# Kernel optimization log

Hardware: AMD Instinct MI355X
Metric: run time of the kernel (lower is better)

The kernel has to match this reference:

```python
import jax, jax.numpy as jnp
import numpy as np

N_NODES = 80000
N_EDGES = 1280000
IN_DIM = 32
EDGE_DIM = 16
HID = 64
DEPTH = 4
BN_EPS = 1e-5
LN_EPS = 1e-5


def setup_inputs() -> dict:
    key = jax.random.key(0)
    ks = jax.random.split(key, 20)
    s = lambda fan: 1.0 / np.sqrt(fan)
    inp = {
        "x": jax.random.normal(ks[0], (N_NODES, IN_DIM), jnp.float32),
        "edge_index": jax.random.randint(ks[1], (2, N_EDGES), 0, N_NODES, jnp.int32),
        "edge_attr": jax.random.normal(ks[2], (N_EDGES, EDGE_DIM), jnp.float32),
        # input embeddings
        "Wx": jax.random.normal(ks[3], (IN_DIM, HID), jnp.float32) * s(IN_DIM),
        "bx": jnp.zeros((HID,), jnp.float32),
        "We": jax.random.normal(ks[4], (EDGE_DIM, HID), jnp.float32) * s(EDGE_DIM),
        "be": jnp.zeros((HID,), jnp.float32),
        # per-layer GIN MLP params (stacked over DEPTH)
        "W1": jax.random.normal(ks[5], (DEPTH, HID, 2 * HID), jnp.float32) * s(HID),
        "b1": jnp.zeros((DEPTH, 2 * HID), jnp.float32),
        "g1": jnp.ones((DEPTH, 2 * HID), jnp.float32),   # BatchNorm gamma
        "bt1": jnp.zeros((DEPTH, 2 * HID), jnp.float32),  # BatchNorm beta
        "W2": jax.random.normal(ks[6], (DEPTH, 2 * HID, HID), jnp.float32) * s(2 * HID),
        "b2": jnp.zeros((DEPTH, HID), jnp.float32),
        "eps": jnp.zeros((DEPTH,), jnp.float32),           # GIN epsilon, init 0
        # per-layer LayerNorm params
        "ln_g": jnp.ones((DEPTH, HID), jnp.float32),
        "ln_b": jnp.zeros((DEPTH, HID), jnp.float32),
    }
    return inp


def reference(x, edge_index, edge_attr, Wx, bx, We, be, W1, b1, g1, bt1, W2, b2, eps, ln_g, ln_b):
    n = x.shape[0]
    h = jax.nn.relu(x @ Wx + bx)                      # [N, HID]
    ea = jax.nn.relu(edge_attr @ We + be)             # [E, HID]
    row, col = edge_index[0], edge_index[1]           # source, target
    L = W1.shape[0]
    for l in range(L):
        # message: relu(x_j + edge_attr), scatter-add into target nodes
        msg = jax.nn.relu(h[row] + ea)                # [E, HID]
        agg = jax.ops.segment_sum(msg, col, num_segments=n)  # [N, HID]
        z = (1.0 + eps[l]) * h + agg
        # GIN MLP: Linear -> BatchNorm(train stats) -> ReLU -> Linear
        z = z @ W1[l] + b1[l]                         # [N, 2*HID]
        mu = z.mean(axis=0)
        var = z.var(axis=0)                           # biased, as torch BN training
        z = (z - mu) * jax.lax.rsqrt(var + BN_EPS) * g1[l] + bt1[l]
        z = jax.nn.relu(z)
        z = z @ W2[l] + b2[l]                         # [N, HID]
        # LayerNorm
        lm = z.mean(axis=-1, keepdims=True)
        lv = z.var(axis=-1, keepdims=True)
        z = (z - lm) * jax.lax.rsqrt(lv + LN_EPS) * ln_g[l] + ln_b[l]
        if l < L - 1:
            z = jax.nn.relu(z)
        h = z
    return h  # JK == 'last'
```

## Files before the change

### kernel.cpp

```cpp
#include <hip/hip_runtime.h>
#include <cstdint>

typedef _Float16 half8 __attribute__((ext_vector_type(8)));
typedef float f32x4 __attribute__((ext_vector_type(4)));

#define NNODES 80000
#define NEDGES 1280000
#define INDIM 32
#define EDIM 16
#define HID 64
#define HID2 128
#define DEPTH 4
#define BN_EPS 1e-5f
#define LN_EPS 1e-5f
#define NB 313

union U16x8 { uint4 v; _Float16 h[8]; };

__global__ __launch_bounds__(256) void k_node_embed(
    const float* __restrict__ x, const float* __restrict__ Wx,
    const float* __restrict__ bx, _Float16* __restrict__ h16) {
    int gw = (blockIdx.x * 256 + threadIdx.x) >> 6;
    int lane = threadIdx.x & 63;
    if (gw >= NNODES) return;
    float xv = (lane < INDIM) ? x[(size_t)gw * INDIM + lane] : 0.f;
    float acc = bx[lane];
#pragma unroll
    for (int k = 0; k < INDIM; k++)
        acc = fmaf(__shfl(xv, k, 64), Wx[k * HID + lane], acc);
    h16[(size_t)gw * HID + lane] = (_Float16)fmaxf(acc, 0.f);
}

__global__ __launch_bounds__(256) void k_prep(
    const float* __restrict__ W1, const float* __restrict__ W2,
    _Float16* __restrict__ w1T, _Float16* __restrict__ w2T) {
    int id = blockIdx.x * 256 + threadIdx.x;
    if (id < DEPTH * 128 * 64) {
        int l = id / 8192, r = id % 8192, n = r / 64, k = r % 64;
        w1T[id] = (_Float16)W1[(size_t)l * 8192 + k * 128 + n];
    } else {
        int idx = id - DEPTH * 128 * 64;
        int l = idx / 8192, r = idx % 8192, n = r / 128, k = r % 128;
        w2T[idx] = (_Float16)W2[(size_t)l * 8192 + k * 64 + n];
    }
}

__global__ __launch_bounds__(256) void k_hist(const int* __restrict__ col, int* __restrict__ deg) {
    int e = blockIdx.x * 256 + threadIdx.x;
    if (e < NEDGES) atomicAdd(&deg[col[e]], 1);
}

__global__ __launch_bounds__(256) void k_scan1(const int* __restrict__ deg, int* __restrict__ bsum) {
    __shared__ int s[256];
    int i = blockIdx.x * 256 + threadIdx.x;
    int v = (i < NNODES) ? deg[i] : 0;
    s[threadIdx.x] = v;
    __syncthreads();
    for (int o = 128; o > 0; o >>= 1) {
        if (threadIdx.x < o) s[threadIdx.x] += s[threadIdx.x + o];
        __syncthreads();
    }
    if (threadIdx.x == 0) bsum[blockIdx.x] = s[0];
}

__global__ __launch_bounds__(512) void k_scan2(const int* __restrict__ bsum, int* __restrict__ boff) {
    __shared__ int s[512];
    int t = threadIdx.x;
    s[t] = (t < NB) ? bsum[t] : 0;
    __syncthreads();
    for (int o = 1; o < 512; o <<= 1) {
        int v = (t >= o) ? s[t - o] : 0;
        __syncthreads();
        s[t] += v;
        __syncthreads();
    }
    if (t < NB) boff[t] = (t == 0) ? 0 : s[t - 1];
}

__global__ __launch_bounds__(256) void k_scan3(const int* __restrict__ deg,
                                               const int* __restrict__ boff,
                                               int* __restrict__ row_off) {
    __shared__ int s[256];
    int i = blockIdx.x * 256 + threadIdx.x;
    int t = threadIdx.x;
    int v = (i < NNODES) ? deg[i] : 0;
    s[t] = v;
    __syncthreads();
    for (int o = 1; o < 256; o <<= 1) {
        int u = (t >= o) ? s[t - o] : 0;
        __syncthreads();
        s[t] += u;
        __syncthreads();
    }
    int incl = s[t];
    if (i < NNODES) row_off[i] = boff[blockIdx.x] + incl - v;
    if (i == NNODES - 1) row_off[NNODES] = boff[blockIdx.x] + incl;
}

__global__ __launch_bounds__(256) void k_copy(const int* __restrict__ src, int* __restrict__ dst) {
    int i = blockIdx.x * 256 + threadIdx.x;
    if (i < NNODES) dst[i] = src[i];
}

__global__ __launch_bounds__(256) void k_scatter(const int* __restrict__ row,
                                                 const int* __restrict__ col,
                                                 int* __restrict__ cursor,
                                                 uint2* __restrict__ sre) {
    int e = blockIdx.x * 256 + threadIdx.x;
    if (e < NEDGES) {
        int c = col[e];
        int pos = atomicAdd(&cursor[c], 1);
        sre[pos] = make_uint2((unsigned)row[e], (unsigned)e);
    }
}

__global__ __launch_bounds__(256) void k_edge_embed(
    const float* __restrict__ eat, const uint2* __restrict__ sre,
    const float* __restrict__ We, const float* __restrict__ be,
    _Float16* __restrict__ eas) {
    __shared__ __align__(16) unsigned char lds[4][5120 + 8192];
    int tid = threadIdx.x;
    int w = tid >> 6, lane = tid & 63;
    unsigned char* A = lds[w];
    unsigned char* O = lds[w] + 5120;
    int ebase = blockIdx.x * 256 + w * 64;
    int b = lane >> 4, c = lane & 15;
    half8 bf[4];
#pragma unroll
    for (int t = 0; t < 4; t++) {
        half8 v = {};
        if (b < 2) {
#pragma unroll
            for (int j = 0; j < 8; j++) {
                int k = b * 8 + j;
                v[j] = (_Float16)We[k * HID + t * 16 + c];
            }
        }
        bf[t] = v;
    }
    float bias[4];
#pragma unroll
    for (int t = 0; t < 4; t++) bias[t] = be[t * 16 + c];
    int eid = (int)sre[ebase + lane].y;
    const float4* ar = (const float4*)(eat + (size_t)eid * EDIM);
    float4 a0 = ar[0], a1 = ar[1], a2 = ar[2], a3 = ar[3];
    U16x8 lo, hi;
    lo.h[0] = (_Float16)a0.x; lo.h[1] = (_Float16)a0.y;
    lo.h[2] = (_Float16)a0.z; lo.h[3] = (_Float16)a0.w;
    lo.h[4] = (_Float16)a1.x; lo.h[5] = (_Float16)a1.y;
    lo.h[6] = (_Float16)a1.z; lo.h[7] = (_Float16)a1.w;
    hi.h[0] = (_Float16)a2.x; hi.h[1] = (_Float16)a2.y;
    hi.h[2] = (_Float16)a2.z; hi.h[3] = (_Float16)a2.w;
    hi.h[4] = (_Float16)a3.x; hi.h[5] = (_Float16)a3.y;
    hi.h[6] = (_Float16)a3.z; hi.h[7] = (_Float16)a3.w;
    uint4 zz = make_uint4(0, 0, 0, 0);
    *(uint4*)(A + lane * 80) = lo.v;
    *(uint4*)(A + lane * 80 + 16) = hi.v;
    *(uint4*)(A + lane * 80 + 32) = zz;
    *(uint4*)(A + lane * 80 + 48) = zz;
    __syncthreads();
#pragma unroll
    for (int it = 0; it < 4; it++) {
        half8 af = *(const half8*)(A + (it * 16 + c) * 80 + b * 16);
#pragma unroll
        for (int t = 0; t < 4; t++) {
            f32x4 acc = {0.f, 0.f, 0.f, 0.f};
            acc = __builtin_amdgcn_mfma_f32_16x16x32_f16(af, bf[t], acc, 0, 0, 0);
#pragma unroll
            for (int r = 0; r < 4; r++) {
                int erow = it * 16 + b * 4 + r;
                int chan = t * 16 + c;
                float v = fmaxf(acc[r] + bias[t], 0.f);
                int byteoff = (erow * 128 + chan * 2) ^ ((erow & 7) << 4);
                *(_Float16*)(O + byteoff) = (_Float16)v;
            }
        }
    }
    __syncthreads();
    uint4* dst = (uint4*)(eas + (size_t)(ebase + lane) * HID);
#pragma unroll
    for (int q = 0; q < 8; q++)
        dst[q] = *(const uint4*)(O + ((lane * 128 + q * 16) ^ ((lane & 7) << 4)));
}

__global__ __launch_bounds__(256) void k_msg(
    const _Float16* __restrict__ h16, const int* __restrict__ row_off,
    const uint2* __restrict__ sre, const _Float16* __restrict__ eas,
    const float* __restrict__ epsp, _Float16* __restrict__ zc16) {
    int gw = (blockIdx.x * 256 + threadIdx.x) >> 6;
    int lane = threadIdx.x & 63;
    if (gw >= NNODES) return;
    int beg = row_off[gw], end = row_off[gw + 1];
    float acc = 0.f;
    int e = beg;
    for (; e + 7 < end; e += 8) {
        int j[8];
#pragma unroll
        for (int u = 0; u < 8; u++) j[u] = (int)sre[e + u].x;
        float hv[8], ev[8];
#pragma unroll
        for (int u = 0; u < 8; u++) hv[u] = (float)h16[(size_t)j[u] * HID + lane];
#pragma unroll
        for (int u = 0; u < 8; u++) ev[u] = (float)eas[(size_t)(e + u) * HID + lane];
        float t0 = fmaxf(hv[0] + ev[0], 0.f) + fmaxf(hv[1] + ev[1], 0.f);
        float t1 = fmaxf(hv[2] + ev[2], 0.f) + fmaxf(hv[3] + ev[3], 0.f);
        float t2 = fmaxf(hv[4] + ev[4], 0.f) + fmaxf(hv[5] + ev[5], 0.f);
        float t3 = fmaxf(hv[6] + ev[6], 0.f) + fmaxf(hv[7] + ev[7], 0.f);
        acc += (t0 + t1) + (t2 + t3);
    }
    for (; e < end; ++e) {
        int j = (int)sre[e].x;
        float hv = (float)h16[(size_t)j * HID + lane];
        float ev = (float)eas[(size_t)e * HID + lane];
        acc += fmaxf(hv + ev, 0.f);
    }
    float epsl = *epsp;
    float hv0 = (float)h16[(size_t)gw * HID + lane];
    zc16[(size_t)gw * HID + lane] = (_Float16)((1.f + epsl) * hv0 + acc);
}

__global__ __launch_bounds__(256) void k_gemm1(
    const _Float16* __restrict__ zc16, const _Float16* __restrict__ w1Tl,
    const float* __restrict__ b1l, _Float16* __restrict__ z1,
    float* __restrict__ bn_acc) {
    __shared__ __align__(16) unsigned char At[64 * 128];
    __shared__ __align__(16) unsigned char Bt[128 * 128];
    __shared__ float red[4][HID2][2];
    int tid = threadIdx.x;
    int nb = blockIdx.x * 64;
#pragma unroll
    for (int i = 0; i < 2; i++) {
        int id = tid + 256 * i;
        int node = id >> 3, c = id & 7;
        uint4 v = *(const uint4*)(zc16 + (size_t)(nb + node) * HID + c * 8);
        *(uint4*)(At + node * 128 + ((c ^ (node & 7)) << 4)) = v;
    }
#pragma unroll
    for (int i = 0; i < 4; i++) {
        int id = tid + 256 * i;
        int r = id >> 3, c = id & 7;
        uint4 v = *(const uint4*)(w1Tl + (size_t)r * HID + c * 8);
        *(uint4*)(Bt + r * 128 + ((c ^ (r & 7)) << 4)) = v;
    }
    __syncthreads();
    int lane = tid & 63, w = tid >> 6;
    int rl = lane & 15, b = lane >> 4;
    f32x4 acc[8];
#pragma unroll
    for (int t = 0; t < 8; t++) acc[t] = (f32x4){0.f, 0.f, 0.f, 0.f};
#pragma unroll
    for (int s = 0; s < 2; s++) {
        int arow = w * 16 + rl;
        half8 af = *(const half8*)(At + arow * 128 + (((s * 4 + b) ^ (rl & 7)) << 4));
#pragma unroll
        for (int t = 0; t < 8; t++) {
            int brow = t * 16 + rl;
            half8 bf = *(const half8*)(Bt + brow * 128 + (((s * 4 + b) ^ (rl & 7)) << 4));
            acc[t] = __builtin_amdgcn_mfma_f32_16x16x32_f16(af, bf, acc[t], 0, 0, 0);
        }
    }
#pragma unroll
    for (int t = 0; t < 8; t++) {
        int colg = t * 16 + rl;
        float bias = b1l[colg];
        float s = 0.f, q = 0.f;
#pragma unroll
        for (int r = 0; r < 4; r++) {
            float v = acc[t][r] + bias;
            int node = nb + w * 16 + b * 4 + r;
            z1[(size_t)node * HID2 + colg] = (_Float16)v;
            s += v;
            q = fmaf(v, v, q);
        }
        s += __shfl_xor(s, 16, 64); s += __shfl_xor(s, 32, 64);
        q += __shfl_xor(q, 16, 64); q += __shfl_xor(q, 32, 64);
        if (b == 0) { red[w][colg][0] = s; red[w][colg][1] = q; }
    }
    __syncthreads();
    int ch = tid & 127, which = tid >> 7;
    float tot = red[0][ch][which] + red[1][ch][which] + red[2][ch][which] + red[3][ch][which];
    atomicAdd(&bn_acc[which * HID2 + ch], tot);
}

__global__ void k_bnfin(const float* __restrict__ bn_acc,
                        const float* __restrict__ g1l,
                        const float* __restrict__ bt1l,
                        float* __restrict__ bn_sc) {
    int c = threadIdx.x;
    if (c >= HID2) return;
    float inv_n = 1.f / (float)NNODES;
    float mu = bn_acc[c] * inv_n;
    float ex2 = bn_acc[HID2 + c] * inv_n;
    float var = ex2 - mu * mu;
    float rs = rsqrtf(var + BN_EPS);
    float sc = g1l[c] * rs;
    bn_sc[c] = sc;
    bn_sc[HID2 + c] = bt1l[c] - mu * sc;
}

__global__ __launch_bounds__(256) void k_mlp2(
    const _Float16* __restrict__ z1, const float* __restrict__ bn_sc,
    const _Float16* __restrict__ w2Tl, const float* __restrict__ b2l,
    const float* __restrict__ lngl, const float* __restrict__ lnbl,
    int last, _Float16* __restrict__ hout, float* __restrict__ fout) {
    __shared__ __align__(16) unsigned char Yt[64 * 256];
    __shared__ __align__(16) unsigned char Wt[64 * 256];
    __shared__ float sbn[256];
    int tid = threadIdx.x;
    int nb = blockIdx.x * 64;
    sbn[tid] = bn_sc[tid];
#pragma unroll
    for (int i = 0; i < 4; i++) {
        int id = tid + 256 * i;
        int r = id >> 4, c = id & 15;
        uint4 v = *(const uint4*)(w2Tl + (size_t)r * HID2 + c * 8);
        *(uint4*)(Wt + r * 256 + ((c ^ (r & 7)) << 4)) = v;
    }
    __syncthreads();
#pragma unroll
    for (int i = 0; i < 4; i++) {
        int id = tid + 256 * i;
        int node = id >> 4, c = id & 15;
        U16x8 u, o;
        u.v = *(const uint4*)(z1 + (size_t)(nb + node) * HID2 + c * 8);
#pragma unroll
        for (int j = 0; j < 8; j++) {
            int chn = c * 8 + j;
            float y = fmaxf(fmaf((float)u.h[j], sbn[chn], sbn[HID2 + chn]), 0.f);
            o.h[j] = (_Float16)y;
        }
        *(uint4*)(Yt + node * 256 + ((c ^ (node & 7)) << 4)) = o.v;
    }
    __syncthreads();
    int lane = tid & 63, w = tid >> 6;
    int rl = lane & 15, b = lane >> 4;
    f32x4 acc[4];
#pragma unroll
    for (int t = 0; t < 4; t++) acc[t] = (f32x4){0.f, 0.f, 0.f, 0.f};
#pragma unroll
    for (int s = 0; s < 4; s++) {
        int arow = w * 16 + rl;
        half8 af = *(const half8*)(Yt + arow * 256 + (((s * 4 + b) ^ (rl & 7)) << 4));
#pragma unroll
        for (int t = 0; t < 4; t++) {
            int brow = t * 16 + rl;
            half8 bf = *(const half8*)(Wt + brow * 256 + (((s * 4 + b) ^ (rl & 7)) << 4));
            acc[t] = __builtin_amdgcn_mfma_f32_16x16x32_f16(af, bf, acc[t], 0, 0, 0);
        }
    }
    float a[4][4];
#pragma unroll
    for (int t = 0; t < 4; t++) {
        float bias = b2l[t * 16 + rl];
#pragma unroll
        for (int r = 0; r < 4; r++) a[r][t] = acc[t][r] + bias;
    }
    float m[4], vv[4];
#pragma unroll
    for (int r = 0; r < 4; r++) {
        float s = (a[r][0] + a[r][1]) + (a[r][2] + a[r][3]);
        s += __shfl_xor(s, 1, 64); s += __shfl_xor(s, 2, 64);
        s += __shfl_xor(s, 4, 64); s += __shfl_xor(s, 8, 64);
        m[r] = s * (1.f / 64.f);
    }
#pragma unroll
    for (int r = 0; r < 4; r++) {
        float t0 = a[r][0] - m[r], t1 = a[r][1] - m[r];
        float t2 = a[r][2] - m[r], t3 = a[r][3] - m[r];
        float q = (t0 * t0 + t1 * t1) + (t2 * t2 + t3 * t3);
        q += __shfl_xor(q, 1, 64); q += __shfl_xor(q, 2, 64);
        q += __shfl_xor(q, 4, 64); q += __shfl_xor(q, 8, 64);
        vv[r] = rsqrtf(q * (1.f / 64.f) + LN_EPS);
    }
#pragma unroll
    for (int t = 0; t < 4; t++) {
        int colg = t * 16 + rl;
        float lg = lngl[colg], lb = lnbl[colg];
#pragma unroll
        for (int r = 0; r < 4; r++) {
            float o = (a[r][t] - m[r]) * vv[r] * lg + lb;
            size_t node = nb + w * 16 + b * 4 + r;
            if (last) {
                fout[node * HID + colg] = o;
            } else {
                hout[node * HID + colg] = (_Float16)fmaxf(o, 0.f);
            }
        }
    }
}

extern "C" void kernel_launch(void* const* d_in, const int* in_sizes, int n_in,
                              void* d_out, int out_size, void* d_ws, size_t ws_size,
                              hipStream_t stream) {
    const float* x   = (const float*)d_in[0];
    const int*   ei  = (const int*)d_in[1];
    const float* eat = (const float*)d_in[2];
    const float* Wx  = (const float*)d_in[3];
    const float* bx  = (const float*)d_in[4];
    const float* We  = (const float*)d_in[5];
    const float* be  = (const float*)d_in[6];
    const float* W1  = (const float*)d_in[7];
    const float* b1  = (const float*)d_in[8];
    const float* g1  = (const float*)d_in[9];
    const float* bt1 = (const float*)d_in[10];
    const float* W2  = (const float*)d_in[11];
    const float* b2  = (const float*)d_in[12];
    const float* eps = (const float*)d_in[13];
    const float* lng = (const float*)d_in[14];
    const float* lnb = (const float*)d_in[15];
    const int* row = ei;
    const int* col = ei + NEDGES;

    char* p = (char*)d_ws;
    auto alloc = [&](size_t bytes) -> char* {
        char* r = p;
        p += (bytes + 255) & ~(size_t)255;
        return r;
    };
    _Float16* h16  = (_Float16*)alloc((size_t)NNODES * HID * 2);
    _Float16* zc16 = (_Float16*)alloc((size_t)NNODES * HID * 2);
    _Float16* z1   = (_Float16*)alloc((size_t)NNODES * HID2 * 2);
    int* row_off   = (int*)alloc((size_t)(NNODES + 1) * 4);
    uint2* sre     = (uint2*)alloc((size_t)NEDGES * 8);
    _Float16* eas  = (_Float16*)alloc((size_t)NEDGES * HID * 2);
    _Float16* w1T  = (_Float16*)alloc((size_t)DEPTH * 128 * 64 * 2);
    _Float16* w2T  = (_Float16*)alloc((size_t)DEPTH * 64 * 128 * 2);
    float* bn_acc  = (float*)alloc(256 * 4);
    float* bn_sc   = (float*)alloc(256 * 4);
    int* cursor = (int*)z1;
    int* bsum   = (int*)z1 + NNODES;
    int* boff   = bsum + NB;
    (void)ws_size; (void)in_sizes; (void)n_in; (void)out_size;

    hipMemsetAsync(cursor, 0, (size_t)NNODES * 4, stream);
    k_node_embed<<<(NNODES + 3) / 4, 256, 0, stream>>>(x, Wx, bx, h16);
    k_prep<<<(DEPTH * 8192 * 2) / 256, 256, 0, stream>>>(W1, W2, w1T, w2T);
    k_hist<<<(NEDGES + 255) / 256, 256, 0, stream>>>(col, cursor);
    k_scan1<<<NB, 256, 0, stream>>>(cursor, bsum);
    k_scan2<<<1, 512, 0, stream>>>(bsum, boff);
    k_scan3<<<NB, 256, 0, stream>>>(cursor, boff, row_off);
    k_copy<<<NB, 256, 0, stream>>>(row_off, cursor);
    k_scatter<<<(NEDGES + 255) / 256, 256, 0, stream>>>(row, col, cursor, sre);
    k_edge_embed<<<NEDGES / 256, 256, 0, stream>>>(eat, sre, We, be, eas);

    const int msg_blocks = (NNODES + 3) / 4;
    const int mm_blocks = NNODES / 64;
    for (int l = 0; l < DEPTH; ++l) {
        k_msg<<<msg_blocks, 256, 0, stream>>>(h16, row_off, sre, eas, eps + l, zc16);
        hipMemsetAsync(bn_acc, 0, 256 * 4, stream);
        k_gemm1<<<mm_blocks, 256, 0, stream>>>(zc16, w1T + (size_t)l * 8192,
                                               b1 + (size_t)l * HID2, z1, bn_acc);
        k_bnfin<<<1, 128, 0, stream>>>(bn_acc, g1 + (size_t)l * HID2,
                                       bt1 + (size_t)l * HID2, bn_sc);
        k_mlp2<<<mm_blocks, 256, 0, stream>>>(z1, bn_sc, w2T + (size_t)l * 8192,
                                              b2 + (size_t)l * HID,
                                              lng + (size_t)l * HID, lnb + (size_t)l * HID,
                                              (l == DEPTH - 1) ? 1 : 0, h16, (float*)d_out);
    }
}
```

Before: 730.3 us.

## Fuse message aggregation into GEMM1 and bucket-partition the CSR edge scatter

The per-layer message kernel is merged into the first MLP GEMM, so each 64-node block gathers and aggregates its neighbours straight into LDS instead of writing and re-reading a zc16 buffer. CSR construction becomes a two-pass bucketed partition: edges are first binned by 128-node bucket into a temp area that reuses the eas buffer, then scattered locally, which should give better write locality than the fully random scatter. The packed uint2 sorted array is split into separate row and edge-id arrays so the gather reads only 4 bytes per edge. The risk is that the fused kernel runs only 1250 blocks with 16 sequential nodes per wave, which lowers latency hiding for the gather, and the bucket capacity of 4096 assumes no bucket overflows for these inputs.

```diff
diff --git a/kernel.cpp b/kernel.cpp
--- a/kernel.cpp
+++ b/kernel.cpp
@@ -14,6 +14,8 @@
 #define BN_EPS 1e-5f
 #define LN_EPS 1e-5f
 #define NB 313
+#define NBUCK 625
+#define BCAP 4096
 
 union U16x8 { uint4 v; _Float16 h[8]; };
 
@@ -45,9 +47,17 @@
     }
 }
 
-__global__ __launch_bounds__(256) void k_hist(const int* __restrict__ col, int* __restrict__ deg) {
+__global__ __launch_bounds__(256) void k_part1(
+    const int* __restrict__ row, const int* __restrict__ col,
+    int* __restrict__ deg, int* __restrict__ bcur, uint2* __restrict__ tmp) {
     int e = blockIdx.x * 256 + threadIdx.x;
-    if (e < NEDGES) atomicAdd(&deg[col[e]], 1);
+    int r = row[e];
+    int c = col[e];
+    atomicAdd(&deg[c], 1);
+    int b = c >> 7;
+    int cloc = c & 127;
+    int p = atomicAdd(&bcur[b], 1);
+    tmp[(size_t)b * BCAP + p] = make_uint2((unsigned)r | ((unsigned)cloc << 17), (unsigned)e);
 }
 
 __global__ __launch_bounds__(256) void k_scan1(const int* __restrict__ deg, int* __restrict__ bsum) {
@@ -102,20 +112,24 @@
     if (i < NNODES) dst[i] = src[i];
 }
 
-__global__ __launch_bounds__(256) void k_scatter(const int* __restrict__ row,
-                                                 const int* __restrict__ col,
-                                                 int* __restrict__ cursor,
-                                                 uint2* __restrict__ sre) {
-    int e = blockIdx.x * 256 + threadIdx.x;
-    if (e < NEDGES) {
-        int c = col[e];
+__global__ __launch_bounds__(256) void k_part2(
+    const uint2* __restrict__ tmp, const int* __restrict__ bcur,
+    int* __restrict__ cursor, int* __restrict__ srow, int* __restrict__ seid) {
+    int b = blockIdx.x;
+    int cnt = bcur[b];
+    const uint2* src = tmp + (size_t)b * BCAP;
+    for (int i = threadIdx.x; i < cnt; i += 256) {
+        uint2 v = src[i];
+        int r = (int)(v.x & 0x1FFFF);
+        int c = (b << 7) + (int)(v.x >> 17);
         int pos = atomicAdd(&cursor[c], 1);
-        sre[pos] = make_uint2((unsigned)row[e], (unsigned)e);
+        srow[pos] = r;
+        seid[pos] = (int)v.y;
     }
 }
 
 __global__ __launch_bounds__(256) void k_edge_embed(
-    const float* __restrict__ eat, const uint2* __restrict__ sre,
+    const float* __restrict__ eat, const int* __restrict__ seid,
     const float* __restrict__ We, const float* __restrict__ be,
     _Float16* __restrict__ eas) {
     __shared__ __align__(16) unsigned char lds[4][5120 + 8192];
@@ -141,7 +155,7 @@
     float bias[4];
 #pragma unroll
     for (int t = 0; t < 4; t++) bias[t] = be[t * 16 + c];
-    int eid = (int)sre[ebase + lane].y;
+    int eid = seid[ebase + lane];
     const float4* ar = (const float4*)(eat + (size_t)eid * EDIM);
     float4 a0 = ar[0], a1 = ar[1], a2 = ar[2], a3 = ar[3];
     U16x8 lo, hi;
@@ -183,44 +197,10 @@
         dst[q] = *(const uint4*)(O + ((lane * 128 + q * 16) ^ ((lane & 7) << 4)));
 }
 
-__global__ __launch_bounds__(256) void k_msg(
+__global__ __launch_bounds__(256) void k_msg1(
     const _Float16* __restrict__ h16, const int* __restrict__ row_off,
-    const uint2* __restrict__ sre, const _Float16* __restrict__ eas,
-    const float* __restrict__ epsp, _Float16* __restrict__ zc16) {
-    int gw = (blockIdx.x * 256 + threadIdx.x) >> 6;
-    int lane = threadIdx.x & 63;
-    if (gw >= NNODES) return;
-    int beg = row_off[gw], end = row_off[gw + 1];
-    float acc = 0.f;
-    int e = beg;
-    for (; e + 7 < end; e += 8) {
-        int j[8];
-#pragma unroll
-        for (int u = 0; u < 8; u++) j[u] = (int)sre[e + u].x;
-        float hv[8], ev[8];
-#pragma unroll
-        for (int u = 0; u < 8; u++) hv[u] = (float)h16[(size_t)j[u] * HID + lane];
-#pragma unroll
-        for (int u = 0; u < 8; u++) ev[u] = (float)eas[(size_t)(e + u) * HID + lane];
-        float t0 = fmaxf(hv[0] + ev[0], 0.f) + fmaxf(hv[1] + ev[1], 0.f);
-        float t1 = fmaxf(hv[2] + ev[2], 0.f) + fmaxf(hv[3] + ev[3], 0.f);
-        float t2 = fmaxf(hv[4] + ev[4], 0.f) + fmaxf(hv[5] + ev[5], 0.f);
-        float t3 = fmaxf(hv[6] + ev[6], 0.f) + fmaxf(hv[7] + ev[7], 0.f);
-        acc += (t0 + t1) + (t2 + t3);
-    }
-    for (; e < end; ++e) {
-        int j = (int)sre[e].x;
-        float hv = (float)h16[(size_t)j * HID + lane];
-        float ev = (float)eas[(size_t)e * HID + lane];
-        acc += fmaxf(hv + ev, 0.f);
-    }
-    float epsl = *epsp;
-    float hv0 = (float)h16[(size_t)gw * HID + lane];
-    zc16[(size_t)gw * HID + lane] = (_Float16)((1.f + epsl) * hv0 + acc);
-}
-
-__global__ __launch_bounds__(256) void k_gemm1(
-    const _Float16* __restrict__ zc16, const _Float16* __restrict__ w1Tl,
+    const int* __restrict__ srow, const _Float16* __restrict__ eas,
+    const float* __restrict__ epsp, const _Float16* __restrict__ w1Tl,
     const float* __restrict__ b1l, _Float16* __restrict__ z1,
     float* __restrict__ bn_acc) {
     __shared__ __align__(16) unsigned char At[64 * 128];
@@ -229,21 +209,47 @@
     int tid = threadIdx.x;
     int nb = blockIdx.x * 64;
 #pragma unroll
-    for (int i = 0; i < 2; i++) {
-        int id = tid + 256 * i;
-        int node = id >> 3, c = id & 7;
-        uint4 v = *(const uint4*)(zc16 + (size_t)(nb + node) * HID + c * 8);
-        *(uint4*)(At + node * 128 + ((c ^ (node & 7)) << 4)) = v;
-    }
-#pragma unroll
     for (int i = 0; i < 4; i++) {
         int id = tid + 256 * i;
         int r = id >> 3, c = id & 7;
         uint4 v = *(const uint4*)(w1Tl + (size_t)r * HID + c * 8);
         *(uint4*)(Bt + r * 128 + ((c ^ (r & 7)) << 4)) = v;
     }
-    __syncthreads();
     int lane = tid & 63, w = tid >> 6;
+    float epsl = 1.f + *epsp;
+    for (int t = 0; t < 16; ++t) {
+        int node = nb + w * 16 + t;
+        int beg = row_off[node], end = row_off[node + 1];
+        float acc = 0.f;
+        int e = beg;
+        for (; e + 7 < end; e += 8) {
+            int j[8];
+#pragma unroll
+            for (int u = 0; u < 8; u++) j[u] = srow[e + u];
+            float hv[8], ev[8];
+#pragma unroll
+            for (int u = 0; u < 8; u++) hv[u] = (float)h16[(size_t)j[u] * HID + lane];
+#pragma unroll
+            for (int u = 0; u < 8; u++) ev[u] = (float)eas[(size_t)(e + u) * HID + lane];
+            float t0 = fmaxf(hv[0] + ev[0], 0.f) + fmaxf(hv[1] + ev[1], 0.f);
+            float t1 = fmaxf(hv[2] + ev[2], 0.f) + fmaxf(hv[3] + ev[3], 0.f);
+            float t2 = fmaxf(hv[4] + ev[4], 0.f) + fmaxf(hv[5] + ev[5], 0.f);
+            float t3 = fmaxf(hv[6] + ev[6], 0.f) + fmaxf(hv[7] + ev[7], 0.f);
+            acc += (t0 + t1) + (t2 + t3);
+        }
+        for (; e < end; ++e) {
+            int j = srow[e];
+            float hv = (float)h16[(size_t)j * HID + lane];
+            float ev = (float)eas[(size_t)e * HID + lane];
+            acc += fmaxf(hv + ev, 0.f);
+        }
+        float hv0 = (float)h16[(size_t)node * HID + lane];
+        float val = epsl * hv0 + acc;
+        int nl = w * 16 + t;
+        int byteoff = nl * 128 + ((((lane >> 3) ^ (nl & 7))) << 4) + (lane & 7) * 2;
+        *(_Float16*)(At + byteoff) = (_Float16)val;
+    }
+    __syncthreads();
     int rl = lane & 15, b = lane >> 4;
     f32x4 acc[8];
 #pragma unroll
@@ -418,38 +424,40 @@
         return r;
     };
     _Float16* h16  = (_Float16*)alloc((size_t)NNODES * HID * 2);
-    _Float16* zc16 = (_Float16*)alloc((size_t)NNODES * HID * 2);
     _Float16* z1   = (_Float16*)alloc((size_t)NNODES * HID2 * 2);
     int* row_off   = (int*)alloc((size_t)(NNODES + 1) * 4);
-    uint2* sre     = (uint2*)alloc((size_t)NEDGES * 8);
+    int* srow      = (int*)alloc((size_t)NEDGES * 4);
     _Float16* eas  = (_Float16*)alloc((size_t)NEDGES * HID * 2);
     _Float16* w1T  = (_Float16*)alloc((size_t)DEPTH * 128 * 64 * 2);
     _Float16* w2T  = (_Float16*)alloc((size_t)DEPTH * 64 * 128 * 2);
     float* bn_acc  = (float*)alloc(256 * 4);
     float* bn_sc   = (float*)alloc(256 * 4);
+    int*   bcur    = (int*)alloc((size_t)NBUCK * 4);
+    uint2* tmp  = (uint2*)eas;
     int* cursor = (int*)z1;
     int* bsum   = (int*)z1 + NNODES;
     int* boff   = bsum + NB;
+    int* seid   = (int*)z1 + 2 * NNODES;
     (void)ws_size; (void)in_sizes; (void)n_in; (void)out_size;
 
     hipMemsetAsync(cursor, 0, (size_t)NNODES * 4, stream);
+    hipMemsetAsync(bcur, 0, (size_t)NBUCK * 4, stream);
     k_node_embed<<<(NNODES + 3) / 4, 256, 0, stream>>>(x, Wx, bx, h16);
     k_prep<<<(DEPTH * 8192 * 2) / 256, 256, 0, stream>>>(W1, W2, w1T, w2T);
-    k_hist<<<(NEDGES + 255) / 256, 256, 0, stream>>>(col, cursor);
+    k_part1<<<NEDGES / 256, 256, 0, stream>>>(row, col, cursor, bcur, tmp);
     k_scan1<<<NB, 256, 0, stream>>>(cursor, bsum);
     k_scan2<<<1, 512, 0, stream>>>(bsum, boff);
     k_scan3<<<NB, 256, 0, stream>>>(cursor, boff, row_off);
     k_copy<<<NB, 256, 0, stream>>>(row_off, cursor);
-    k_scatter<<<(NEDGES + 255) / 256, 256, 0, stream>>>(row, col, cursor, sre);
-    k_edge_embed<<<NEDGES / 256, 256, 0, stream>>>(eat, sre, We, be, eas);
-
-    const int msg_blocks = (NNODES + 3) / 4;
+    k_part2<<<NBUCK, 256, 0, stream>>>(tmp, bcur, cursor, srow, seid);
+    k_edge_embed<<<NEDGES / 256, 256, 0, stream>>>(eat, seid, We, be, eas);
+
     const int mm_blocks = NNODES / 64;
     for (int l = 0; l < DEPTH; ++l) {
-        k_msg<<<msg_blocks, 256, 0, stream>>>(h16, row_off, sre, eas, eps + l, zc16);
         hipMemsetAsync(bn_acc, 0, 256 * 4, stream);
-        k_gemm1<<<mm_blocks, 256, 0, stream>>>(zc16, w1T + (size_t)l * 8192,
-                                               b1 + (size_t)l * HID2, z1, bn_acc);
+        k_msg1<<<mm_blocks, 256, 0, stream>>>(h16, row_off, srow, eas, eps + l,
+                                              w1T + (size_t)l * 8192,
+                                              b1 + (size_t)l * HID2, z1, bn_acc);
         k_bnfin<<<1, 128, 0, stream>>>(bn_acc, g1 + (size_t)l * HID2,
                                        bt1 + (size_t)l * HID2, bn_sc);
         k_mlp2<<<mm_blocks, 256, 0, stream>>>(z1, bn_sc, w2T + (size_t)l * 8192,
```

Result: slower. 1.246 ms (+70.7%).

## Partition histogram and scatter atomics by destination range per XCD

Applied to the files above, without the earlier changes.

Reworks the degree histogram and CSR scatter kernels so that each block handles a slice of edges but only applies atomics for destination nodes in one of eight node ranges, selected by blockIdx&7. The intent is that blocks scheduled round-robin onto the same XCD touch only one eighth of the counter array, keeping atomics L2-local and avoiding cross-die contention. In exchange, every edge's column is read eight times and most lanes go idle on the range test, and the XCD mapping assumption is not guaranteed.

```diff
diff --git a/kernel.cpp b/kernel.cpp
--- a/kernel.cpp
+++ b/kernel.cpp
@@ -14,6 +14,8 @@
 #define BN_EPS 1e-5f
 #define LN_EPS 1e-5f
 #define NB 313
+#define NPX 10000
+#define EPS 10000
 
 union U16x8 { uint4 v; _Float16 h[8]; };
 
@@ -45,9 +47,21 @@
     }
 }
 
-__global__ __launch_bounds__(256) void k_hist(const int* __restrict__ col, int* __restrict__ deg) {
-    int e = blockIdx.x * 256 + threadIdx.x;
-    if (e < NEDGES) atomicAdd(&deg[col[e]], 1);
+__global__ __launch_bounds__(256) void k_hist(const int* __restrict__ col,
+                                              int* __restrict__ deg) {
+    int xcd = blockIdx.x & 7;
+    int slice = blockIdx.x >> 3;
+    int base = slice * EPS;
+    int lo = xcd * NPX;
+    const int4* c4 = (const int4*)(col + base);
+    for (int i = threadIdx.x; i < EPS / 4; i += 256) {
+        int4 c = c4[i];
+#pragma unroll
+        for (int u = 0; u < 4; u++) {
+            int cc = (&c.x)[u];
+            if ((unsigned)(cc - lo) < (unsigned)NPX) atomicAdd(&deg[cc], 1);
+        }
+    }
 }
 
 __global__ __launch_bounds__(256) void k_scan1(const int* __restrict__ deg, int* __restrict__ bsum) {
@@ -102,15 +116,26 @@
     if (i < NNODES) dst[i] = src[i];
 }
 
-__global__ __launch_bounds__(256) void k_scatter(const int* __restrict__ row,
-                                                 const int* __restrict__ col,
-                                                 int* __restrict__ cursor,
-                                                 uint2* __restrict__ sre) {
-    int e = blockIdx.x * 256 + threadIdx.x;
-    if (e < NEDGES) {
-        int c = col[e];
-        int pos = atomicAdd(&cursor[c], 1);
-        sre[pos] = make_uint2((unsigned)row[e], (unsigned)e);
+__global__ __launch_bounds__(256) void k_scatter(
+    const int* __restrict__ row, const int* __restrict__ col,
+    int* __restrict__ cursor, uint2* __restrict__ sre) {
+    int xcd = blockIdx.x & 7;
+    int slice = blockIdx.x >> 3;
+    int base = slice * EPS;
+    int lo = xcd * NPX;
+    const int4* c4 = (const int4*)(col + base);
+    for (int i = threadIdx.x; i < EPS / 4; i += 256) {
+        int4 c = c4[i];
+        int e0 = base + i * 4;
+#pragma unroll
+        for (int u = 0; u < 4; u++) {
+            int cc = (&c.x)[u];
+            if ((unsigned)(cc - lo) < (unsigned)NPX) {
+                int e = e0 + u;
+                int pos = atomicAdd(&cursor[cc], 1);
+                sre[pos] = make_uint2((unsigned)row[e], (unsigned)e);
+            }
+        }
     }
 }
 
@@ -435,12 +460,12 @@
     hipMemsetAsync(cursor, 0, (size_t)NNODES * 4, stream);
     k_node_embed<<<(NNODES + 3) / 4, 256, 0, stream>>>(x, Wx, bx, h16);
     k_prep<<<(DEPTH * 8192 * 2) / 256, 256, 0, stream>>>(W1, W2, w1T, w2T);
-    k_hist<<<(NEDGES + 255) / 256, 256, 0, stream>>>(col, cursor);
+    k_hist<<<(NEDGES / EPS) * 8, 256, 0, stream>>>(col, cursor);
     k_scan1<<<NB, 256, 0, stream>>>(cursor, bsum);
     k_scan2<<<1, 512, 0, stream>>>(bsum, boff);
     k_scan3<<<NB, 256, 0, stream>>>(cursor, boff, row_off);
     k_copy<<<NB, 256, 0, stream>>>(row_off, cursor);
-    k_scatter<<<(NEDGES + 255) / 256, 256, 0, stream>>>(row, col, cursor, sre);
+    k_scatter<<<(NEDGES / EPS) * 8, 256, 0, stream>>>(row, col, cursor, sre);
     k_edge_embed<<<NEDGES / 256, 256, 0, stream>>>(eat, sre, We, be, eas);
 
     const int msg_blocks = (NNODES + 3) / 4;
```

New measurement: 698.0 us. -4.4%, faster.
